# Kernel tuning notes

Hardware: AMD Instinct MI355X
Metric: run time of the kernel (lower is better)

Reference implementation:

```python
import jax, jax.numpy as jnp
import numpy as np

KK = 9  # 3x3 kernel points
PAD = 1
EPS = 1e-5


def _conv2d(x, w, b):
    # x: [B,C,H,W], w: [O,I,3,3]
    y = jax.lax.conv_general_dilated(
        x, w, window_strides=(1, 1), padding=((PAD, PAD), (PAD, PAD)),
        dimension_numbers=("NCHW", "OIHW", "NCHW"))
    return y + b[None, :, None, None]


def _bilinear_sample_one(img, py, px):
    # img: [C,H,W]; py, px: [KK,H,W] fractional sample coords
    C, H, W = img.shape
    y0 = jnp.floor(py).astype(jnp.int32)
    x0 = jnp.floor(px).astype(jnp.int32)
    wy = py - y0
    wx = px - x0

    def g(yi, xi):
        ok = ((yi >= 0) & (yi < H) & (xi >= 0) & (xi < W)).astype(img.dtype)
        v = img[:, jnp.clip(yi, 0, H - 1), jnp.clip(xi, 0, W - 1)]  # [C,KK,H,W]
        return v * ok[None]

    v00 = g(y0, x0)
    v01 = g(y0, x0 + 1)
    v10 = g(y0 + 1, x0)
    v11 = g(y0 + 1, x0 + 1)
    return (v00 * (1 - wy) * (1 - wx) + v01 * (1 - wy) * wx
            + v10 * wy * (1 - wx) + v11 * wy * wx)  # [C,KK,H,W]


def setup_inputs() -> dict:
    key = jax.random.key(0)
    ks = jax.random.split(key, 8)
    B, C, H, W = 8, 256, 96, 96
    O = 256
    x = jax.random.normal(ks[0], (B, C, H, W), dtype=jnp.float32)
    # modulated DCNv2 offset/mask conv: 3*KK output channels
    w_off = jax.random.normal(ks[1], (3 * KK, C, 3, 3), dtype=jnp.float32) * 0.01
    b_off = jnp.zeros((3 * KK,), dtype=jnp.float32)
    w_dcn = jax.random.normal(ks[2], (O, C, 3, 3), dtype=jnp.float32) * (1.0 / np.sqrt(C * KK))
    b_dcn = jnp.zeros((O,), dtype=jnp.float32)
    gamma = jnp.ones((O,), dtype=jnp.float32)
    beta = jnp.zeros((O,), dtype=jnp.float32)
    running_mean = jax.random.normal(ks[3], (O,), dtype=jnp.float32) * 0.1
    running_var = jax.random.uniform(ks[4], (O,), dtype=jnp.float32, minval=0.5, maxval=1.5)
    return {"x": x, "w_off": w_off, "b_off": b_off, "w_dcn": w_dcn,
            "b_dcn": b_dcn, "gamma": gamma, "beta": beta,
            "running_mean": running_mean, "running_var": running_var}


def reference(x, w_off, b_off, w_dcn, b_dcn, gamma, beta, running_mean, running_var):
    B, C, H, W = x.shape
    O = w_dcn.shape[0]
    # offsets + modulation masks
    om = _conv2d(x, w_off, b_off)                  # [B, 3*KK, H, W]
    offset = om[:, :2 * KK]
    mask = jax.nn.sigmoid(om[:, 2 * KK:])          # [B, KK, H, W]
    off_y = offset[:, 0::2]                        # [B, KK, H, W]
    off_x = offset[:, 1::2]

    ky, kx = jnp.meshgrid(jnp.arange(3), jnp.arange(3), indexing="ij")
    ky = ky.reshape(KK).astype(x.dtype)
    kx = kx.reshape(KK).astype(x.dtype)
    hh = jnp.arange(H, dtype=x.dtype)
    ww = jnp.arange(W, dtype=x.dtype)
    # fractional sampling coordinates per output pixel per kernel point
    py = off_y + hh[None, None, :, None] + ky[None, :, None, None] - PAD
    px = off_x + ww[None, None, None, :] + kx[None, :, None, None] - PAD

    sampled = jax.vmap(_bilinear_sample_one)(x, py, px)  # [B,C,KK,H,W]
    sampled = sampled * mask[:, None]
    out = jnp.einsum("bckhw,ock->bohw", sampled, w_dcn.reshape(O, C, KK))
    out = out + b_dcn[None, :, None, None]
    # BatchNorm (inference, running stats) + ReLU
    inv = jax.lax.rsqrt(running_var + EPS)
    out = (out - running_mean[None, :, None, None]) * (gamma * inv)[None, :, None, None]
    out = out + beta[None, :, None, None]
    return jax.nn.relu(out)
```

## Files before the change

### kernel.cpp

```cpp
#include <hip/hip_runtime.h>
#include <hip/hip_bf16.h>
#include <cstdint>
#include <cstddef>

#define H 96
#define W 96
#define HW 9216
#define C 256
#define B 8
#define O 256
#define KK 9
#define EPS 1e-5f

typedef __attribute__((ext_vector_type(8))) short short8;
typedef __attribute__((ext_vector_type(4))) float float4v;
typedef unsigned short ushort_t;
typedef unsigned int uint_t;

__global__ __launch_bounds__(256) void transpose_x_k(
    const float* __restrict__ x, ushort_t* __restrict__ xt)
{
    __shared__ float tile[64][65];
    int t = threadIdx.x;
    int p0 = blockIdx.x * 64;
    int c0 = blockIdx.y * 64;
    int b  = blockIdx.z;
    {
        int tx = t & 63, ty = t >> 6;
        const float* xb = x + ((size_t)b * C + c0 + ty) * HW + p0 + tx;
#pragma unroll
        for (int i = 0; i < 64; i += 4)
            tile[ty + i][tx] = xb[(size_t)i * HW];
    }
    __syncthreads();
    {
        int tc = t & 31, tp = t >> 5;
        ushort_t* xtb = xt + ((size_t)b * HW + p0) * C + c0;
#pragma unroll
        for (int i = 0; i < 64; i += 8) {
            int p = tp + i;
            float a  = tile[2 * tc][p];
            float bb = tile[2 * tc + 1][p];
            __hip_bfloat162 h2 = __float22bfloat162_rn(make_float2(a, bb));
            uint_t u;
            __builtin_memcpy(&u, &h2, 4);
            *reinterpret_cast<uint_t*>(&xtb[(size_t)p * C + 2 * tc]) = u;
        }
    }
}

__global__ __launch_bounds__(256) void prep_b_k(
    const float* __restrict__ wd, ushort_t* __restrict__ bp)
{
    int idx = blockIdx.x * 256 + threadIdx.x;
    int kk = idx / (O * C);
    int r = idx - kk * O * C;
    int o = r >> 8, c = r & 255;
    float v = wd[((size_t)o * C + c) * KK + kk];
    __hip_bfloat16 hh = __float2bfloat16(v);
    ushort_t u;
    __builtin_memcpy(&u, &hh, 2);
    bp[idx] = u;
}

__global__ __launch_bounds__(256) void prep_bo_k(
    const float* __restrict__ wo, ushort_t* __restrict__ bo)
{
    int idx = blockIdx.x * 256 + threadIdx.x;
    int n = idx / (KK * C);
    int r = idx - n * KK * C;
    int kk = r >> 8, c = r & 255;
    float v = (n < 27) ? wo[((size_t)n * C + c) * KK + kk] : 0.0f;
    __hip_bfloat16 hh = __float2bfloat16(v);
    ushort_t u;
    __builtin_memcpy(&u, &hh, 2);
    bo[idx] = u;
}

__global__ __launch_bounds__(256) void offset_mfma_k(
    const ushort_t* __restrict__ xt, const ushort_t* __restrict__ bo,
    const float* __restrict__ b_off, float* __restrict__ om)
{
    int t = threadIdx.x;
    int wv = t >> 6, l = t & 63;
    int ln = l & 15, lq = l >> 4;
    int d = blockIdx.x;
    int lb = (d & 7) * 72 + (d >> 3);
    int p0 = lb * 128;
    int b = p0 / HW;
    int rem0w = p0 - b * HW + wv * 32;
    const ushort_t* xtb = xt + (size_t)b * HW * C;

    int hh0[2], ww0[2];
#pragma unroll
    for (int mt = 0; mt < 2; ++mt) {
        int rem = rem0w + mt * 16 + ln;
        hh0[mt] = rem / W;
        ww0[mt] = rem - hh0[mt] * W;
    }

    float4v acc[2][2];
#pragma unroll
    for (int i = 0; i < 2; ++i)
#pragma unroll
        for (int j = 0; j < 2; ++j) acc[i][j] = (float4v){0.f, 0.f, 0.f, 0.f};

#pragma unroll
    for (int kk = 0; kk < KK; ++kk) {
        int dy = kk / 3 - 1, dx = kk % 3 - 1;
        const ushort_t* ap[2];
        uint_t msk[2];
#pragma unroll
        for (int mt = 0; mt < 2; ++mt) {
            int hh = hh0[mt] + dy, ww = ww0[mt] + dx;
            bool ok = (hh >= 0) & (hh < H) & (ww >= 0) & (ww < W);
            msk[mt] = ok ? 0xffffffffu : 0u;
            int hc = min(max(hh, 0), H - 1);
            int wc = min(max(ww, 0), W - 1);
            ap[mt] = xtb + (size_t)(hc * W + wc) * C + lq * 8;
        }
        const ushort_t* bp0 = bo + ((size_t)(0 * 16 + ln) * KK + kk) * C + lq * 8;
        const ushort_t* bp1 = bo + ((size_t)(1 * 16 + ln) * KK + kk) * C + lq * 8;
#pragma unroll
        for (int cc = 0; cc < 8; ++cc) {
            int c0 = cc * 32;
            short8 af[2];
#pragma unroll
            for (int mt = 0; mt < 2; ++mt) {
                uint4 u = *(const uint4*)(ap[mt] + c0);
                u.x &= msk[mt]; u.y &= msk[mt]; u.z &= msk[mt]; u.w &= msk[mt];
                __builtin_memcpy(&af[mt], &u, 16);
            }
            short8 bf0 = *(const short8*)(bp0 + c0);
            short8 bf1 = *(const short8*)(bp1 + c0);
#pragma unroll
            for (int mt = 0; mt < 2; ++mt) {
                acc[mt][0] = __builtin_amdgcn_mfma_f32_16x16x32_bf16(af[mt], bf0, acc[mt][0], 0, 0, 0);
                acc[mt][1] = __builtin_amdgcn_mfma_f32_16x16x32_bf16(af[mt], bf1, acc[mt][1], 0, 0, 0);
            }
        }
    }

    float* omb = om + (size_t)b * 27 * HW + rem0w;
#pragma unroll
    for (int nt = 0; nt < 2; ++nt) {
        int oc = nt * 16 + ln;
        if (oc < 27) {
            float bv = b_off[oc];
            float* po = omb + (size_t)oc * HW + lq * 4;
#pragma unroll
            for (int mt = 0; mt < 2; ++mt) {
                float4 v;
                v.x = acc[mt][nt].x + bv;
                v.y = acc[mt][nt].y + bv;
                v.z = acc[mt][nt].z + bv;
                v.w = acc[mt][nt].w + bv;
                *(float4*)(po + mt * 16) = v;
            }
        }
    }
}

__device__ __forceinline__ void unpack8(uint4 q, float* v) {
    v[0] = __uint_as_float(q.x << 16);
    v[1] = __uint_as_float(q.x & 0xffff0000u);
    v[2] = __uint_as_float(q.y << 16);
    v[3] = __uint_as_float(q.y & 0xffff0000u);
    v[4] = __uint_as_float(q.z << 16);
    v[5] = __uint_as_float(q.z & 0xffff0000u);
    v[6] = __uint_as_float(q.w << 16);
    v[7] = __uint_as_float(q.w & 0xffff0000u);
}

__device__ __forceinline__ uint_t packbf2(float a, float b) {
    __hip_bfloat162 h2 = __float22bfloat162_rn(make_float2(a, b));
    uint_t u;
    __builtin_memcpy(&u, &h2, 4);
    return u;
}

__global__ __launch_bounds__(256) void dcn_main_k(
    const ushort_t* __restrict__ xt, const float* __restrict__ om,
    const ushort_t* __restrict__ bp, const float* __restrict__ b_dcn,
    const float* __restrict__ gamma, const float* __restrict__ beta,
    const float* __restrict__ rmean, const float* __restrict__ rvar,
    float* __restrict__ out)
{
    __shared__ uint4    s_rec0[64 * KK];
    __shared__ float2   s_rec1[64 * KK];
    __shared__ ushort_t s_a[2][2][64][32];

    int t = threadIdx.x;
    int d = blockIdx.x;
    int lb = (d & 7) * 144 + (d >> 3);
    int p0 = lb * 64;
    int b = p0 / HW;
    int rem0 = p0 - b * HW;

    for (int v = t; v < 64 * KK; v += 256) {
        int m = v & 63;
        int k = v >> 6;
        int rem = rem0 + m;
        int h = rem / W;
        int w = rem - h * W;
        const float* omb = om + (size_t)b * 27 * HW + rem;
        float offy = omb[(size_t)(2 * k) * HW];
        float offx = omb[(size_t)(2 * k + 1) * HW];
        float z    = omb[(size_t)(18 + k) * HW];
        float mval = 1.0f / (1.0f + __expf(-z));
        float py = (float)(h + k / 3 - 1) + offy;
        float px = (float)(w + k % 3 - 1) + offx;
        float fy = floorf(py), fx = floorf(px);
        int y0 = (int)fy, x0 = (int)fx;
        float wy = py - fy, wx = px - fx;
        float row0f = (1.0f - wy) * mval * ((y0 >= 0 && y0 < H) ? 1.0f : 0.0f);
        float row1f = wy * mval * ((y0 >= -1 && y0 < H - 1) ? 1.0f : 0.0f);
        int xsel = min(max(x0, 0), W - 2);
        float wxa = (x0 >= 0 && x0 < W) ? (1.0f - wx) : 0.0f;
        float wxb = (x0 >= -1 && x0 < W - 1) ? wx : 0.0f;
        int cx0 = min(max(x0, 0), W - 1);
        int cx1 = min(max(x0 + 1, 0), W - 1);
        float wA = ((cx0 == xsel) ? wxa : 0.0f) + ((cx1 == xsel) ? wxb : 0.0f);
        float wB = ((cx0 == xsel + 1) ? wxa : 0.0f) + ((cx1 == xsel + 1) ? wxb : 0.0f);
        int yc0 = min(max(y0, 0), H - 1);
        int yc1 = min(max(y0 + 1, 0), H - 1);
        uint4 r0;
        r0.x = (uint_t)((yc0 * W + xsel) * C);
        r0.y = (uint_t)((yc1 * W + xsel) * C);
        r0.z = __float_as_uint(row0f * wA);
        r0.w = __float_as_uint(row0f * wB);
        s_rec0[v] = r0;
        s_rec1[v] = make_float2(row1f * wA, row1f * wB);
    }

    float4v acc[4][4];
#pragma unroll
    for (int i = 0; i < 4; ++i)
#pragma unroll
        for (int j = 0; j < 4; ++j)
            acc[i][j] = (float4v){0.f, 0.f, 0.f, 0.f};

    const ushort_t* xtb = xt + (size_t)b * HW * C;
    int wv = t >> 6;
    int l  = t & 63;
    int ln = l & 15;
    int lq = l >> 4;
    int sm = t >> 2;
    int sc = (t & 3) * 8;

    __syncthreads();

    uint4 L[8];
    float Wt[4];

#define ISSUE_A(it_) do {                                                   \
        int kk_ = (it_) >> 2, q_ = (it_) & 3;                               \
        uint4 r0_ = s_rec0[kk_ * 64 + sm];                                  \
        float2 r1_ = s_rec1[kk_ * 64 + sm];                                 \
        const ushort_t* a0_ = xtb + r0_.x + q_ * 64 + sc;                   \
        const ushort_t* a1_ = xtb + r0_.y + q_ * 64 + sc;                   \
        Wt[0] = __uint_as_float(r0_.z); Wt[1] = __uint_as_float(r0_.w);     \
        Wt[2] = r1_.x; Wt[3] = r1_.y;                                       \
        L[0] = *(const uint4*)(a0_);      L[1] = *(const uint4*)(a0_ + C);  \
        L[2] = *(const uint4*)(a1_);      L[3] = *(const uint4*)(a1_ + C);  \
        L[4] = *(const uint4*)(a0_ + 32); L[5] = *(const uint4*)(a0_ + C + 32); \
        L[6] = *(const uint4*)(a1_ + 32); L[7] = *(const uint4*)(a1_ + C + 32); \
    } while (0)

#define COMBINE_WRITE(db_) do {                                             \
        _Pragma("unroll")                                                   \
        for (int j_ = 0; j_ < 2; ++j_) {                                    \
            float v0_[8], v1_[8], v2_[8], v3_[8], val_[8];                  \
            unpack8(L[j_ * 4 + 0], v0_); unpack8(L[j_ * 4 + 1], v1_);       \
            unpack8(L[j_ * 4 + 2], v2_); unpack8(L[j_ * 4 + 3], v3_);       \
            _Pragma("unroll")                                               \
            for (int e_ = 0; e_ < 8; ++e_)                                  \
                val_[e_] = v0_[e_] * Wt[0] + v1_[e_] * Wt[1]                \
                         + v2_[e_] * Wt[2] + v3_[e_] * Wt[3];               \
            uint4 pk_;                                                      \
            pk_.x = packbf2(val_[0], val_[1]);                              \
            pk_.y = packbf2(val_[2], val_[3]);                              \
            pk_.z = packbf2(val_[4], val_[5]);                              \
            pk_.w = packbf2(val_[6], val_[7]);                              \
            *(uint4*)&s_a[db_][j_][sm][sc] = pk_;                           \
        }                                                                   \
    } while (0)

    ISSUE_A(0);
    COMBINE_WRITE(0);

    for (int it = 0; it < 36; ++it) {
        int kk = it >> 2, q = it & 3;
        int buf = it & 1;
        __syncthreads();

        if (it < 35) ISSUE_A(it + 1);

        const ushort_t* bpk = bp + ((size_t)kk * O + wv * 64 + ln) * C + q * 64 + lq * 8;
#pragma unroll
        for (int j = 0; j < 2; ++j) {
            short8 af[4], bfr[4];
#pragma unroll
            for (int nt = 0; nt < 4; ++nt)
                bfr[nt] = *(const short8*)(bpk + (size_t)nt * 16 * C + j * 32);
#pragma unroll
            for (int mt = 0; mt < 4; ++mt)
                af[mt] = *(const short8*)&s_a[buf][j][mt * 16 + ln][lq * 8];
#pragma unroll
            for (int mt = 0; mt < 4; ++mt)
#pragma unroll
                for (int nt = 0; nt < 4; ++nt)
                    acc[mt][nt] = __builtin_amdgcn_mfma_f32_16x16x32_bf16(
                        af[mt], bfr[nt], acc[mt][nt], 0, 0, 0);
        }

        if (it < 35) COMBINE_WRITE(buf ^ 1);
    }
#undef ISSUE_A
#undef COMBINE_WRITE

#pragma unroll
    for (int nt = 0; nt < 4; ++nt) {
        int o = wv * 64 + nt * 16 + ln;
        float scale = gamma[o] * rsqrtf(rvar[o] + EPS);
        float shift = (b_dcn[o] - rmean[o]) * scale + beta[o];
        float* po = out + ((size_t)b * O + o) * HW + rem0 + lq * 4;
#pragma unroll
        for (int mt = 0; mt < 4; ++mt) {
            float4 vv;
            vv.x = fmaxf(acc[mt][nt].x * scale + shift, 0.0f);
            vv.y = fmaxf(acc[mt][nt].y * scale + shift, 0.0f);
            vv.z = fmaxf(acc[mt][nt].z * scale + shift, 0.0f);
            vv.w = fmaxf(acc[mt][nt].w * scale + shift, 0.0f);
            *(float4*)(po + mt * 16) = vv;
        }
    }
}

extern "C" void kernel_launch(void* const* d_in, const int* in_sizes, int n_in,
                              void* d_out, int out_size, void* d_ws, size_t ws_size,
                              hipStream_t stream) {
    const float* x     = (const float*)d_in[0];
    const float* w_off = (const float*)d_in[1];
    const float* b_off = (const float*)d_in[2];
    const float* w_dcn = (const float*)d_in[3];
    const float* b_dcn = (const float*)d_in[4];
    const float* gamma = (const float*)d_in[5];
    const float* beta  = (const float*)d_in[6];
    const float* rmean = (const float*)d_in[7];
    const float* rvar  = (const float*)d_in[8];
    float* out = (float*)d_out;

    float*    om  = (float*)d_ws;
    ushort_t* bpw = (ushort_t*)(om + (size_t)B * 27 * HW);
    ushort_t* bow = bpw + (size_t)KK * O * C;
    ushort_t* xtw = bow + (size_t)32 * KK * C;

    hipLaunchKernelGGL(transpose_x_k, dim3(144, 4, 8), dim3(256), 0, stream,
                       x, xtw);
    hipLaunchKernelGGL(prep_b_k, dim3(2304), dim3(256), 0, stream,
                       w_dcn, bpw);
    hipLaunchKernelGGL(prep_bo_k, dim3(288), dim3(256), 0, stream,
                       w_off, bow);
    hipLaunchKernelGGL(offset_mfma_k, dim3(73728 / 128), dim3(256), 0, stream,
                       xtw, bow, b_off, om);
    hipLaunchKernelGGL(dcn_main_k, dim3(73728 / 64), dim3(256), 0, stream,
                       xtw, om, bpw, b_dcn, gamma, beta, rmean, rvar, out);
}
```

Baseline: 476.8 us.

## Restructure DCN main loop to stage full channel slab per kernel point

The main loop now runs per kernel point (9 steps) instead of 36 quarter-channel steps. Each step stages all 256 channels of bilinear-combined samples in an enlarged double-buffered LDS tile and needs only one block barrier per step instead of one per quarter. The gathers and combines for the next kernel point are interleaved with the MFMAs on the current one. Weight fragments are software-prefetched one chunk ahead, and the bf16 unpack-combine uses 2-wide float vectors. LDS use grows from 16KB to 64KB for the A tile, which may reduce occupancy, and register pressure rises.

```diff
diff --git a/kernel.cpp b/kernel.cpp
--- a/kernel.cpp
+++ b/kernel.cpp
@@ -14,6 +14,7 @@
 
 typedef __attribute__((ext_vector_type(8))) short short8;
 typedef __attribute__((ext_vector_type(4))) float float4v;
+typedef __attribute__((ext_vector_type(2))) float float2v;
 typedef unsigned short ushort_t;
 typedef unsigned int uint_t;
 
@@ -161,15 +162,11 @@
     }
 }
 
-__device__ __forceinline__ void unpack8(uint4 q, float* v) {
-    v[0] = __uint_as_float(q.x << 16);
-    v[1] = __uint_as_float(q.x & 0xffff0000u);
-    v[2] = __uint_as_float(q.y << 16);
-    v[3] = __uint_as_float(q.y & 0xffff0000u);
-    v[4] = __uint_as_float(q.z << 16);
-    v[5] = __uint_as_float(q.z & 0xffff0000u);
-    v[6] = __uint_as_float(q.w << 16);
-    v[7] = __uint_as_float(q.w & 0xffff0000u);
+__device__ __forceinline__ float2v up2(uint_t u) {
+    float2v r;
+    r.x = __uint_as_float(u << 16);
+    r.y = __uint_as_float(u & 0xffff0000u);
+    return r;
 }
 
 __device__ __forceinline__ uint_t packbf2(float a, float b) {
@@ -188,7 +185,7 @@
 {
     __shared__ uint4    s_rec0[64 * KK];
     __shared__ float2   s_rec1[64 * KK];
-    __shared__ ushort_t s_a[2][2][64][32];
+    __shared__ ushort_t s_a[2][8][64][32];
 
     int t = threadIdx.x;
     int d = blockIdx.x;
@@ -250,74 +247,96 @@
 
     __syncthreads();
 
-    uint4 L[8];
-    float Wt[4];
-
-#define ISSUE_A(it_) do {                                                   \
-        int kk_ = (it_) >> 2, q_ = (it_) & 3;                               \
-        uint4 r0_ = s_rec0[kk_ * 64 + sm];                                  \
-        float2 r1_ = s_rec1[kk_ * 64 + sm];                                 \
-        const ushort_t* a0_ = xtb + r0_.x + q_ * 64 + sc;                   \
-        const ushort_t* a1_ = xtb + r0_.y + q_ * 64 + sc;                   \
-        Wt[0] = __uint_as_float(r0_.z); Wt[1] = __uint_as_float(r0_.w);     \
-        Wt[2] = r1_.x; Wt[3] = r1_.y;                                       \
-        L[0] = *(const uint4*)(a0_);      L[1] = *(const uint4*)(a0_ + C);  \
-        L[2] = *(const uint4*)(a1_);      L[3] = *(const uint4*)(a1_ + C);  \
-        L[4] = *(const uint4*)(a0_ + 32); L[5] = *(const uint4*)(a0_ + C + 32); \
-        L[6] = *(const uint4*)(a1_ + 32); L[7] = *(const uint4*)(a1_ + C + 32); \
+#define COMBINE(L0_, L1_, L2_, L3_, W_, dst_) do {                          \
+        uint4 pk_;                                                          \
+        float2v r0_ = up2((L0_).x) * (W_)[0] + up2((L1_).x) * (W_)[1]       \
+                    + up2((L2_).x) * (W_)[2] + up2((L3_).x) * (W_)[3];      \
+        float2v r1_ = up2((L0_).y) * (W_)[0] + up2((L1_).y) * (W_)[1]       \
+                    + up2((L2_).y) * (W_)[2] + up2((L3_).y) * (W_)[3];      \
+        float2v r2_ = up2((L0_).z) * (W_)[0] + up2((L1_).z) * (W_)[1]       \
+                    + up2((L2_).z) * (W_)[2] + up2((L3_).z) * (W_)[3];      \
+        float2v r3_ = up2((L0_).w) * (W_)[0] + up2((L1_).w) * (W_)[1]       \
+                    + up2((L2_).w) * (W_)[2] + up2((L3_).w) * (W_)[3];      \
+        pk_.x = packbf2(r0_.x, r0_.y);                                      \
+        pk_.y = packbf2(r1_.x, r1_.y);                                      \
+        pk_.z = packbf2(r2_.x, r2_.y);                                      \
+        pk_.w = packbf2(r3_.x, r3_.y);                                      \
+        *(uint4*)(dst_) = pk_;                                              \
     } while (0)
 
-#define COMBINE_WRITE(db_) do {                                             \
-        _Pragma("unroll")                                                   \
-        for (int j_ = 0; j_ < 2; ++j_) {                                    \
-            float v0_[8], v1_[8], v2_[8], v3_[8], val_[8];                  \
-            unpack8(L[j_ * 4 + 0], v0_); unpack8(L[j_ * 4 + 1], v1_);       \
-            unpack8(L[j_ * 4 + 2], v2_); unpack8(L[j_ * 4 + 3], v3_);       \
-            _Pragma("unroll")                                               \
-            for (int e_ = 0; e_ < 8; ++e_)                                  \
-                val_[e_] = v0_[e_] * Wt[0] + v1_[e_] * Wt[1]                \
-                         + v2_[e_] * Wt[2] + v3_[e_] * Wt[3];               \
-            uint4 pk_;                                                      \
-            pk_.x = packbf2(val_[0], val_[1]);                              \
-            pk_.y = packbf2(val_[2], val_[3]);                              \
-            pk_.z = packbf2(val_[4], val_[5]);                              \
-            pk_.w = packbf2(val_[6], val_[7]);                              \
-            *(uint4*)&s_a[db_][j_][sm][sc] = pk_;                           \
-        }                                                                   \
-    } while (0)
-
-    ISSUE_A(0);
-    COMBINE_WRITE(0);
-
-    for (int it = 0; it < 36; ++it) {
-        int kk = it >> 2, q = it & 3;
-        int buf = it & 1;
-        __syncthreads();
-
-        if (it < 35) ISSUE_A(it + 1);
-
-        const ushort_t* bpk = bp + ((size_t)kk * O + wv * 64 + ln) * C + q * 64 + lq * 8;
-#pragma unroll
-        for (int j = 0; j < 2; ++j) {
-            short8 af[4], bfr[4];
-#pragma unroll
-            for (int nt = 0; nt < 4; ++nt)
-                bfr[nt] = *(const short8*)(bpk + (size_t)nt * 16 * C + j * 32);
+    {
+        uint4 r0 = s_rec0[sm];
+        float2 r1 = s_rec1[sm];
+        const ushort_t* a0 = xtb + r0.x + sc;
+        const ushort_t* a1 = xtb + r0.y + sc;
+        float Wt[4] = {__uint_as_float(r0.z), __uint_as_float(r0.w), r1.x, r1.y};
+#pragma unroll
+        for (int ci = 0; ci < 8; ++ci) {
+            uint4 L0 = *(const uint4*)(a0 + ci * 32);
+            uint4 L1 = *(const uint4*)(a0 + ci * 32 + C);
+            uint4 L2 = *(const uint4*)(a1 + ci * 32);
+            uint4 L3 = *(const uint4*)(a1 + ci * 32 + C);
+            COMBINE(L0, L1, L2, L3, Wt, &s_a[0][ci][sm][sc]);
+        }
+    }
+    __syncthreads();
+
+    for (int kk = 0; kk < KK; ++kk) {
+        int rb = kk & 1;
+        int wb = rb ^ 1;
+        bool more = (kk < KK - 1);
+
+        const ushort_t* a0n = xtb;
+        const ushort_t* a1n = xtb;
+        float Wn[4] = {0.f, 0.f, 0.f, 0.f};
+        if (more) {
+            uint4 r0 = s_rec0[(kk + 1) * 64 + sm];
+            float2 r1 = s_rec1[(kk + 1) * 64 + sm];
+            a0n = xtb + r0.x + sc;
+            a1n = xtb + r0.y + sc;
+            Wn[0] = __uint_as_float(r0.z); Wn[1] = __uint_as_float(r0.w);
+            Wn[2] = r1.x; Wn[3] = r1.y;
+        }
+
+        const ushort_t* bpk = bp + ((size_t)kk * O + wv * 64 + ln) * C + lq * 8;
+        short8 bfr[4], bfrN[4];
+#pragma unroll
+        for (int nt = 0; nt < 4; ++nt)
+            bfr[nt] = *(const short8*)(bpk + (size_t)nt * 16 * C);
+
+#pragma unroll
+        for (int ci = 0; ci < 8; ++ci) {
+            uint4 L0, L1, L2, L3;
+            if (more) {
+                L0 = *(const uint4*)(a0n + ci * 32);
+                L1 = *(const uint4*)(a0n + ci * 32 + C);
+                L2 = *(const uint4*)(a1n + ci * 32);
+                L3 = *(const uint4*)(a1n + ci * 32 + C);
+            }
+            if (ci < 7) {
+#pragma unroll
+                for (int nt = 0; nt < 4; ++nt)
+                    bfrN[nt] = *(const short8*)(bpk + (size_t)nt * 16 * C + (ci + 1) * 32);
+            }
+            short8 af[4];
 #pragma unroll
             for (int mt = 0; mt < 4; ++mt)
-                af[mt] = *(const short8*)&s_a[buf][j][mt * 16 + ln][lq * 8];
+                af[mt] = *(const short8*)&s_a[rb][ci][mt * 16 + ln][lq * 8];
 #pragma unroll
             for (int mt = 0; mt < 4; ++mt)
 #pragma unroll
                 for (int nt = 0; nt < 4; ++nt)
                     acc[mt][nt] = __builtin_amdgcn_mfma_f32_16x16x32_bf16(
                         af[mt], bfr[nt], acc[mt][nt], 0, 0, 0);
-        }
-
-        if (it < 35) COMBINE_WRITE(buf ^ 1);
-    }
-#undef ISSUE_A
-#undef COMBINE_WRITE
+            if (more)
+                COMBINE(L0, L1, L2, L3, Wn, &s_a[wb][ci][sm][sc]);
+#pragma unroll
+            for (int nt = 0; nt < 4; ++nt)
+                bfr[nt] = bfrN[nt];
+        }
+        __syncthreads();
+    }
+#undef COMBINE
 
 #pragma unroll
     for (int nt = 0; nt < 4; ++nt) {
```

After: 459.0 us. -3.7%, faster.
